# Kernel optimization log

Hardware: AMD Instinct MI355X
Metric: run time of the kernel (lower is better)

Reference implementation:

```python
import jax, jax.numpy as jnp
import numpy as np

MODEL_DIM = 1024
TOTAL_DIM = 1024
N_HEADS = 16
HEAD_DIM = TOTAL_DIM // N_HEADS


def setup_inputs() -> dict:
    key = jax.random.key(0)
    k1, k2, k3 = jax.random.split(key, 3)
    query = jax.random.normal(k1, (2, 2048, MODEL_DIM), dtype=jnp.float32)
    # nn.Linear(model_dim, 3*total_dim, bias=False): store as [in, out] for x @ W
    W_in = jax.random.normal(k2, (MODEL_DIM, 3 * TOTAL_DIM), dtype=jnp.float32) / np.sqrt(MODEL_DIM)
    W_out = jax.random.normal(k3, (TOTAL_DIM, MODEL_DIM), dtype=jnp.float32) / np.sqrt(TOTAL_DIM)
    return {"query": query, "W_in": W_in, "W_out": W_out}


def reference(query, W_in, W_out):
    B, S, _ = query.shape
    qkv = query @ W_in                      # [B, S, 3*D]
    q, k, v = jnp.split(qkv, 3, axis=-1)    # each [B, S, D]

    def to_heads(t):
        return t.reshape(B, S, N_HEADS, HEAD_DIM).transpose(0, 2, 1, 3)  # [B,H,S,d]

    q, k, v = to_heads(q), to_heads(k), to_heads(v)
    scale = 1.0 / np.sqrt(HEAD_DIM).astype(np.float32)
    scores = jnp.einsum('bhqd,bhkd->bhqk', q, k) * scale  # [B,H,S,S]
    causal = jnp.tril(jnp.ones((S, S), dtype=bool))
    scores = jnp.where(causal, scores, jnp.finfo(scores.dtype).min)
    probs = jax.nn.softmax(scores, axis=-1)
    attn = jnp.einsum('bhqk,bhkd->bhqd', probs, v)        # [B,H,S,d]
    attn = attn.transpose(0, 2, 1, 3).reshape(B, S, TOTAL_DIM)
    return attn @ W_out                     # [B, S, model_dim]
```

## Files before the change

kernel.cpp:

```cpp
#include <hip/hip_runtime.h>


typedef __bf16 bf16x8 __attribute__((ext_vector_type(8)));
typedef __bf16 bf16x4 __attribute__((ext_vector_type(4)));
typedef short s16x4 __attribute__((ext_vector_type(4)));
typedef float f32x4 __attribute__((ext_vector_type(4)));
typedef int i32x2 __attribute__((ext_vector_type(2)));

#define B_   2
#define S_   2048
#define DM   1024
#define NH   16
#define HD   64
#define N3   3072
#define M_   4096

#define SCALE_LOG2E 0.180336884f

__device__ __forceinline__ unsigned short f2bf(float f) {
  unsigned int u = __float_as_uint(f);
  u += 0x7fffu + ((u >> 16) & 1u);
  return (unsigned short)(u >> 16);
}

__device__ __forceinline__ void gload_lds16(void* lds, const void* g) {
  __builtin_amdgcn_global_load_lds(
      (__attribute__((address_space(1))) void*)g,
      (__attribute__((address_space(3))) void*)lds, 16, 0, 0);
}

__device__ __forceinline__ f32x4 mfma16(bf16x4 a, bf16x4 b, f32x4 c) {
#if __has_builtin(__builtin_amdgcn_mfma_f32_16x16x16_bf16)
  return __builtin_amdgcn_mfma_f32_16x16x16_bf16(a, b, c, 0, 0, 0);
#else
  return __builtin_amdgcn_mfma_f32_16x16x16bf16_1k(
      __builtin_bit_cast(s16x4, a), __builtin_bit_cast(s16x4, b), c, 0, 0, 0);
#endif
}

__device__ __forceinline__ int cvtpk(float s0, float s1) {
  int r;
  asm("v_cvt_pk_bf16_f32 %0, %1, %2" : "=v"(r) : "v"(s0), "v"(s1));
  return r;
}

__global__ __launch_bounds__(256) void f32_to_bf16_vec(
    const float4* __restrict__ in, unsigned short* __restrict__ out, int n4) {
  int i = blockIdx.x * 256 + threadIdx.x;
  if (i < n4) {
    float4 v = in[i];
    ushort4 o;
    o.x = f2bf(v.x); o.y = f2bf(v.y); o.z = f2bf(v.z); o.w = f2bf(v.w);
    *(ushort4*)(&out[(size_t)i * 4]) = o;
  }
}

__global__ __launch_bounds__(256) void transpose_f32_bf16(
    const float* __restrict__ in, unsigned short* __restrict__ out, int R, int C,
    int scale_rows, float scale) {
  __shared__ float tile[32][33];
  const int tx = threadIdx.x, ty = threadIdx.y;
  const int x = blockIdx.x * 32 + tx;
  const int y0 = blockIdx.y * 32;
#pragma unroll
  for (int j = 0; j < 32; j += 8)
    tile[ty + j][tx] = in[(size_t)(y0 + ty + j) * C + x];
  __syncthreads();
  const int ox = y0 + tx;
  const int oy0 = blockIdx.x * 32;
#pragma unroll
  for (int j = 0; j < 32; j += 8) {
    const int orow = oy0 + ty + j;
    float v = tile[tx][ty + j];
    if (orow < scale_rows) v *= scale;
    out[(size_t)orow * R + ox] = f2bf(v);
  }
}

__global__ __launch_bounds__(256) void transpose_v(
    const unsigned short* __restrict__ qkv, unsigned short* __restrict__ vTn) {
  __shared__ unsigned short tile[64][72];
  const int kt = blockIdx.x;
  const int h  = blockIdx.y;
  const int b  = blockIdx.z;
  const int t  = threadIdx.x;
  const int row = t >> 3;
  const int c8  = (t & 7) * 8;
#pragma unroll
  for (int rr = 0; rr < 2; rr++) {
    const int s = row + rr * 32;
    const size_t src = (size_t)(b * S_ + kt * 64 + s) * N3 + 2 * DM + h * HD + c8;
    *(float4*)&tile[s][c8] = *(const float4*)&qkv[src];
  }
  __syncthreads();
  const size_t base = (size_t)((b * NH + h) * 32 + kt) * 4096;
#pragma unroll
  for (int u0 = 0; u0 < 2; u0++) {
    const int u = t + u0 * 256;
    const int p = u >> 8, d = (u >> 2) & 63, q = u & 3;
    const int s0 = 32 * p + q * 4;
    ushort4 w0, w1;
    w0.x = tile[s0 + 0][d];  w0.y = tile[s0 + 1][d];
    w0.z = tile[s0 + 2][d];  w0.w = tile[s0 + 3][d];
    w1.x = tile[s0 + 16][d]; w1.y = tile[s0 + 17][d];
    w1.z = tile[s0 + 18][d]; w1.w = tile[s0 + 19][d];
    *(ushort4*)&vTn[base + (size_t)u * 8]     = w0;
    *(ushort4*)&vTn[base + (size_t)u * 8 + 4] = w1;
  }
}

template <int OUT_BF16>
__global__ __launch_bounds__(256) void gemm_abt(
    const unsigned short* __restrict__ A, const unsigned short* __restrict__ Bt,
    void* __restrict__ Cv, int M, int N, int K) {
  __shared__ __align__(16) unsigned short a_sm[128 * 32];
  __shared__ __align__(16) unsigned short b_sm[128 * 32];
  const int tid = threadIdx.x;
  const int lane = tid & 63, wave = tid >> 6;
  const int quad = lane >> 4, l15 = lane & 15;
  const int row0 = blockIdx.y * 128, col0 = blockIdx.x * 128;
  const int wm = (wave >> 1) * 64, wn = (wave & 1) * 64;

  f32x4 acc[4][4];
#pragma unroll
  for (int i = 0; i < 4; i++)
#pragma unroll
    for (int j = 0; j < 4; j++) acc[i][j] = (f32x4){0.f, 0.f, 0.f, 0.f};

  const int e0 = tid * 8;

  for (int k0 = 0; k0 < K; k0 += 32) {
    __syncthreads();
#pragma unroll
    for (int i = 0; i < 2; i++) {
      int e = e0 + i * 2048;
      int r = e >> 5, c = e & 31;
      gload_lds16(&a_sm[e], &A[(size_t)(row0 + r) * K + k0 + c]);
      gload_lds16(&b_sm[e], &Bt[(size_t)(col0 + r) * K + k0 + c]);
    }
    __syncthreads();

    bf16x8 af[4], bfb[4];
#pragma unroll
    for (int i = 0; i < 4; i++) {
      af[i]  = *(const bf16x8*)&a_sm[(wm + i * 16 + l15) * 32 + quad * 8];
      bfb[i] = *(const bf16x8*)&b_sm[(wn + i * 16 + l15) * 32 + quad * 8];
    }
#pragma unroll
    for (int i = 0; i < 4; i++)
#pragma unroll
      for (int j = 0; j < 4; j++)
        acc[i][j] = __builtin_amdgcn_mfma_f32_16x16x32_bf16(af[i], bfb[j], acc[i][j], 0, 0, 0);
  }

#pragma unroll
  for (int i = 0; i < 4; i++) {
#pragma unroll
    for (int j = 0; j < 4; j++) {
#pragma unroll
      for (int r = 0; r < 4; r++) {
        const int row = row0 + wm + i * 16 + quad * 4 + r;
        const int col = col0 + wn + j * 16 + l15;
        const float v = acc[i][j][r];
        if (OUT_BF16)
          ((unsigned short*)Cv)[(size_t)row * N + col] = f2bf(v);
        else
          ((float*)Cv)[(size_t)row * N + col] = v;
      }
    }
  }
}

__global__ __launch_bounds__(256) void gemm_abt_64(
    const unsigned short* __restrict__ A, const unsigned short* __restrict__ Bt,
    float* __restrict__ C, int M, int N, int K) {
  __shared__ __align__(16) unsigned short a_sm[64 * 32];
  __shared__ __align__(16) unsigned short b_sm[128 * 32];
  const int tid = threadIdx.x;
  const int lane = tid & 63, wave = tid >> 6;
  const int quad = lane >> 4, l15 = lane & 15;
  const int row0 = blockIdx.y * 64, col0 = blockIdx.x * 128;
  const int wn = wave * 32;

  f32x4 acc[4][2];
#pragma unroll
  for (int i = 0; i < 4; i++)
#pragma unroll
    for (int j = 0; j < 2; j++) acc[i][j] = (f32x4){0.f, 0.f, 0.f, 0.f};

  const int e0 = tid * 8;

  for (int k0 = 0; k0 < K; k0 += 32) {
    __syncthreads();
    {
      const int r = e0 >> 5, c = e0 & 31;
      gload_lds16(&a_sm[e0], &A[(size_t)(row0 + r) * K + k0 + c]);
    }
#pragma unroll
    for (int i = 0; i < 2; i++) {
      int e = e0 + i * 2048;
      int r = e >> 5, c = e & 31;
      gload_lds16(&b_sm[e], &Bt[(size_t)(col0 + r) * K + k0 + c]);
    }
    __syncthreads();

    bf16x8 af[4], bfb[2];
#pragma unroll
    for (int i = 0; i < 4; i++)
      af[i] = *(const bf16x8*)&a_sm[(i * 16 + l15) * 32 + quad * 8];
#pragma unroll
    for (int j = 0; j < 2; j++)
      bfb[j] = *(const bf16x8*)&b_sm[(wn + j * 16 + l15) * 32 + quad * 8];
#pragma unroll
    for (int i = 0; i < 4; i++)
#pragma unroll
      for (int j = 0; j < 2; j++)
        acc[i][j] = __builtin_amdgcn_mfma_f32_16x16x32_bf16(af[i], bfb[j], acc[i][j], 0, 0, 0);
  }

#pragma unroll
  for (int i = 0; i < 4; i++) {
#pragma unroll
    for (int j = 0; j < 2; j++) {
#pragma unroll
      for (int r = 0; r < 4; r++) {
        const int row = row0 + i * 16 + quad * 4 + r;
        const int col = col0 + wn + j * 16 + l15;
        C[(size_t)row * N + col] = acc[i][j][r];
      }
    }
  }
}

__global__ __launch_bounds__(512, 4) void attn_fused12(
    const unsigned short* __restrict__ qkv,
    const unsigned short* __restrict__ vTn,
    unsigned short* __restrict__ attnout) {
  const int h = blockIdx.y, b = blockIdx.z;
  const int j = blockIdx.x;
  const int tid = threadIdx.x;
  const int lane = tid & 63, wave = tid >> 6;
  const int quad = lane >> 4, l15 = lane & 15;
  const int sw = l15 & 7;

  __shared__ __align__(16) unsigned short k_sm[4 * 4096];
  __shared__ __align__(16) unsigned short vt_sm[4 * 4096];

  const int wrow0 = (wave < 4) ? (j * 64 + wave * 16)
                               : ((31 - j) * 64 + (wave - 4) * 16);
  const int qrow = wrow0 + l15;

  bf16x8 qf[2];
  {
    const unsigned short* qp = qkv + (size_t)(b * S_ + qrow) * N3 + h * HD + quad * 8;
    qf[0] = *(const bf16x8*)qp;
    qf[1] = *(const bf16x8*)(qp + 32);
  }

  f32x4 o[4];
#pragma unroll
  for (int n = 0; n < 4; n++) o[n] = (f32x4){0.f, 0.f, 0.f, 0.f};
  float lsum = 0.f;

  const int r0s = tid >> 3;
  const int gch = ((tid & 7) ^ (r0s & 7)) * 8;
  const unsigned short* kgb = qkv + (size_t)(b * S_ + r0s) * N3 + DM + h * HD + gch;
  const unsigned short* vgl = vTn + (size_t)((b * NH + h) * 32) * 4096 + tid * 8;

  const int nt = 32 - j;

  int pk[4][2];
  const unsigned short* vbp = &vt_sm[0];

  auto PV = [&]() {
    __builtin_amdgcn_s_setprio(1);
#pragma unroll
    for (int p = 0; p < 2; p++) {
      i32x2 wlo, whi;
      wlo.x = pk[2 * p][0];     wlo.y = pk[2 * p][1];
      whi.x = pk[2 * p + 1][0]; whi.y = pk[2 * p + 1][1];
      const bf16x4 blo = __builtin_bit_cast(bf16x4, wlo);
      const bf16x4 bhi = __builtin_bit_cast(bf16x4, whi);
#pragma unroll
      for (int mb = 0; mb < 4; mb++) {
        const bf16x8 vv =
            *(const bf16x8*)&vbp[(p * 256 + mb * 64 + l15 * 4 + quad) * 8];
        bf16x4 alo, ahi;
#pragma unroll
        for (int i = 0; i < 4; i++) { alo[i] = vv[i]; ahi[i] = vv[i + 4]; }
        o[mb] = mfma16(alo, blo, o[mb]);
        o[mb] = mfma16(ahi, bhi, o[mb]);
      }
    }
    __builtin_amdgcn_s_setprio(0);
  };

  gload_lds16(&k_sm[tid * 8], kgb);
  gload_lds16(&vt_sm[tid * 8], vgl);
  gload_lds16(&k_sm[4096 + tid * 8], kgb + (size_t)64 * N3);
  gload_lds16(&vt_sm[4096 + tid * 8], vgl + 4096);

  for (int t = 0; t < nt; t++) {
    if (t + 1 < nt) asm volatile("s_waitcnt vmcnt(2)" ::: "memory");
    else            asm volatile("s_waitcnt vmcnt(0)" ::: "memory");
    __builtin_amdgcn_s_barrier();
    __builtin_amdgcn_sched_barrier(0);
    if (t + 2 < nt) {
      const int b2 = (t + 2) & 3;
      gload_lds16(&k_sm[b2 * 4096 + tid * 8], kgb + (size_t)(t + 2) * 64 * N3);
      gload_lds16(&vt_sm[b2 * 4096 + tid * 8], vgl + (size_t)(t + 2) * 4096);
    }
    const unsigned short* kb = &k_sm[(t & 3) * 4096];
    const unsigned short* vb = &vt_sm[(t & 3) * 4096];

    if (t >= 1 && (t - 1) * 64 <= wrow0 + 15) PV();

    if (t * 64 <= wrow0 + 15) {
      f32x4 s[4];
#pragma unroll
      for (int mb = 0; mb < 4; mb++) s[mb] = (f32x4){0.f, 0.f, 0.f, 0.f};
      __builtin_amdgcn_s_setprio(1);
#pragma unroll
      for (int mb = 0; mb < 4; mb++) {
        const int ro = (mb * 16 + l15) * 64;
        bf16x8 kf0 = *(const bf16x8*)&kb[ro + ((quad ^ sw) << 3)];
        bf16x8 kf1 = *(const bf16x8*)&kb[ro + (((4 + quad) ^ sw) << 3)];
        s[mb] = __builtin_amdgcn_mfma_f32_16x16x32_bf16(kf0, qf[0], s[mb], 0, 0, 0);
        s[mb] = __builtin_amdgcn_mfma_f32_16x16x32_bf16(kf1, qf[1], s[mb], 0, 0, 0);
      }
      __builtin_amdgcn_s_setprio(0);

      if (t * 64 + 63 <= wrow0) {
#pragma unroll
        for (int mb = 0; mb < 4; mb++)
#pragma unroll
          for (int r = 0; r < 4; r++)
            s[mb][r] = exp2f(s[mb][r]);
      } else {
        const int kq0 = t * 64 + quad * 4;
#pragma unroll
        for (int mb = 0; mb < 4; mb++)
#pragma unroll
          for (int r = 0; r < 4; r++) {
            const float e = exp2f(s[mb][r]);
            s[mb][r] = (kq0 + mb * 16 + r <= qrow) ? e : 0.f;
          }
      }
#pragma unroll
      for (int mb = 0; mb < 4; mb++)
        lsum += (s[mb][0] + s[mb][1]) + (s[mb][2] + s[mb][3]);

#pragma unroll
      for (int mb = 0; mb < 4; mb++) {
        pk[mb][0] = cvtpk(s[mb][0], s[mb][1]);
        pk[mb][1] = cvtpk(s[mb][2], s[mb][3]);
      }
      vbp = vb;
    }
  }

  if ((nt - 1) * 64 <= wrow0 + 15) PV();

  asm volatile("s_waitcnt vmcnt(0)" ::: "memory");

  float l = lsum;
  l += __shfl_xor(l, 16);
  l += __shfl_xor(l, 32);
  const float inv = 1.0f / l;
  const size_t grow = (size_t)(b * S_ + qrow);
#pragma unroll
  for (int mb = 0; mb < 4; mb++) {
    ushort4 w;
    w.x = f2bf(o[mb][0] * inv);
    w.y = f2bf(o[mb][1] * inv);
    w.z = f2bf(o[mb][2] * inv);
    w.w = f2bf(o[mb][3] * inv);
    *(ushort4*)&attnout[grow * DM + h * HD + mb * 16 + quad * 4] = w;
  }
}

extern "C" void kernel_launch(void* const* d_in, const int* in_sizes, int n_in,
                              void* d_out, int out_size, void* d_ws, size_t ws_size,
                              hipStream_t stream) {
  const float* query = (const float*)d_in[0];
  const float* w_in  = (const float*)d_in[1];
  const float* w_out = (const float*)d_in[2];
  float* out = (float*)d_out;

  char* ws = (char*)d_ws;
  unsigned short* qbf     = (unsigned short*)(ws);
  unsigned short* vTn     = (unsigned short*)(ws);
  unsigned short* w_in_t  = (unsigned short*)(ws + 8388608);
  unsigned short* w_out_t = (unsigned short*)(ws + 14680064);
  unsigned short* qkv     = (unsigned short*)(ws + 16777216);
  unsigned short* attn    = (unsigned short*)(ws + 41943040);

  f32_to_bf16_vec<<<dim3(M_ * DM / 1024), dim3(256), 0, stream>>>(
      (const float4*)query, qbf, M_ * DM / 4);
  transpose_f32_bf16<<<dim3(N3 / 32, DM / 32), dim3(32, 8), 0, stream>>>(
      w_in, w_in_t, DM, N3, DM, SCALE_LOG2E);
  transpose_f32_bf16<<<dim3(DM / 32, DM / 32), dim3(32, 8), 0, stream>>>(
      w_out, w_out_t, DM, DM, 0, 1.0f);
  gemm_abt<1><<<dim3(N3 / 128, M_ / 128), dim3(256), 0, stream>>>(qbf, w_in_t, qkv, M_, N3, DM);
  transpose_v<<<dim3(32, NH, B_), dim3(256), 0, stream>>>(qkv, vTn);
  attn_fused12<<<dim3(16, NH, B_), dim3(512), 0, stream>>>(qkv, vTn, attn);
  gemm_abt_64<<<dim3(DM / 128, M_ / 64), dim3(256), 0, stream>>>(attn, w_out_t, out, M_, DM, DM);
}
```

Baseline: 194.6 us.

## Merge prep kernels and write V transposed directly from QKV GEMM epilogue

Combines the query cast and both weight transposes into a single prep launch that dispatches on block index. The QKV GEMM epilogue now writes the V section straight into the blocked transposed layout used by attention, so the separate transpose_v kernel and its read-back of V are gone. Workspace offsets are reshuffled so attn reuses the qbf region and vTn gets its own buffer. This saves two launches and a V round trip through memory, at the cost of scattered 8-byte stores in the GEMM epilogue.

```diff
diff --git a/kernel.cpp b/kernel.cpp
--- a/kernel.cpp
+++ b/kernel.cpp
@@ -44,75 +44,54 @@
   return r;
 }
 
-__global__ __launch_bounds__(256) void f32_to_bf16_vec(
-    const float4* __restrict__ in, unsigned short* __restrict__ out, int n4) {
-  int i = blockIdx.x * 256 + threadIdx.x;
-  if (i < n4) {
-    float4 v = in[i];
+__global__ __launch_bounds__(256) void prep(
+    const float* __restrict__ query, const float* __restrict__ w_in,
+    const float* __restrict__ w_out, unsigned short* __restrict__ qbf,
+    unsigned short* __restrict__ w_in_t, unsigned short* __restrict__ w_out_t) {
+  __shared__ float tile[32][33];
+  const int bx = blockIdx.x;
+  const int t = threadIdx.x;
+  if (bx < 4096) {
+    const int i = bx * 256 + t;
+    const float4 v = ((const float4*)query)[i];
     ushort4 o;
     o.x = f2bf(v.x); o.y = f2bf(v.y); o.z = f2bf(v.z); o.w = f2bf(v.w);
-    *(ushort4*)(&out[(size_t)i * 4]) = o;
-  }
-}
-
-__global__ __launch_bounds__(256) void transpose_f32_bf16(
-    const float* __restrict__ in, unsigned short* __restrict__ out, int R, int C,
-    int scale_rows, float scale) {
-  __shared__ float tile[32][33];
-  const int tx = threadIdx.x, ty = threadIdx.y;
-  const int x = blockIdx.x * 32 + tx;
-  const int y0 = blockIdx.y * 32;
+    *(ushort4*)(&qbf[(size_t)i * 4]) = o;
+    return;
+  }
+  const int tx = t & 31, ty = t >> 5;
+  const float* in;
+  unsigned short* out;
+  int R, C, bxx, bxy, scale_rows;
+  if (bx < 4096 + 3072) {
+    const int id = bx - 4096;
+    in = w_in; out = w_in_t; R = DM; C = N3;
+    bxx = id % 96; bxy = id / 96; scale_rows = DM;
+  } else {
+    const int id = bx - 7168;
+    in = w_out; out = w_out_t; R = DM; C = DM;
+    bxx = id & 31; bxy = id >> 5; scale_rows = 0;
+  }
+  const int x = bxx * 32 + tx;
+  const int y0 = bxy * 32;
 #pragma unroll
   for (int j = 0; j < 32; j += 8)
     tile[ty + j][tx] = in[(size_t)(y0 + ty + j) * C + x];
   __syncthreads();
   const int ox = y0 + tx;
-  const int oy0 = blockIdx.x * 32;
+  const int oy0 = bxx * 32;
 #pragma unroll
   for (int j = 0; j < 32; j += 8) {
     const int orow = oy0 + ty + j;
     float v = tile[tx][ty + j];
-    if (orow < scale_rows) v *= scale;
+    if (orow < scale_rows) v *= SCALE_LOG2E;
     out[(size_t)orow * R + ox] = f2bf(v);
   }
 }
 
-__global__ __launch_bounds__(256) void transpose_v(
-    const unsigned short* __restrict__ qkv, unsigned short* __restrict__ vTn) {
-  __shared__ unsigned short tile[64][72];
-  const int kt = blockIdx.x;
-  const int h  = blockIdx.y;
-  const int b  = blockIdx.z;
-  const int t  = threadIdx.x;
-  const int row = t >> 3;
-  const int c8  = (t & 7) * 8;
-#pragma unroll
-  for (int rr = 0; rr < 2; rr++) {
-    const int s = row + rr * 32;
-    const size_t src = (size_t)(b * S_ + kt * 64 + s) * N3 + 2 * DM + h * HD + c8;
-    *(float4*)&tile[s][c8] = *(const float4*)&qkv[src];
-  }
-  __syncthreads();
-  const size_t base = (size_t)((b * NH + h) * 32 + kt) * 4096;
-#pragma unroll
-  for (int u0 = 0; u0 < 2; u0++) {
-    const int u = t + u0 * 256;
-    const int p = u >> 8, d = (u >> 2) & 63, q = u & 3;
-    const int s0 = 32 * p + q * 4;
-    ushort4 w0, w1;
-    w0.x = tile[s0 + 0][d];  w0.y = tile[s0 + 1][d];
-    w0.z = tile[s0 + 2][d];  w0.w = tile[s0 + 3][d];
-    w1.x = tile[s0 + 16][d]; w1.y = tile[s0 + 17][d];
-    w1.z = tile[s0 + 18][d]; w1.w = tile[s0 + 19][d];
-    *(ushort4*)&vTn[base + (size_t)u * 8]     = w0;
-    *(ushort4*)&vTn[base + (size_t)u * 8 + 4] = w1;
-  }
-}
-
-template <int OUT_BF16>
-__global__ __launch_bounds__(256) void gemm_abt(
+__global__ __launch_bounds__(256) void gemm_qkv(
     const unsigned short* __restrict__ A, const unsigned short* __restrict__ Bt,
-    void* __restrict__ Cv, int M, int N, int K) {
+    unsigned short* __restrict__ qkv, unsigned short* __restrict__ vTn) {
   __shared__ __align__(16) unsigned short a_sm[128 * 32];
   __shared__ __align__(16) unsigned short b_sm[128 * 32];
   const int tid = threadIdx.x;
@@ -120,6 +99,7 @@
   const int quad = lane >> 4, l15 = lane & 15;
   const int row0 = blockIdx.y * 128, col0 = blockIdx.x * 128;
   const int wm = (wave >> 1) * 64, wn = (wave & 1) * 64;
+  const int K = DM;
 
   f32x4 acc[4][4];
 #pragma unroll
@@ -153,19 +133,39 @@
         acc[i][j] = __builtin_amdgcn_mfma_f32_16x16x32_bf16(af[i], bfb[j], acc[i][j], 0, 0, 0);
   }
 
-#pragma unroll
-  for (int i = 0; i < 4; i++) {
-#pragma unroll
-    for (int j = 0; j < 4; j++) {
-#pragma unroll
-      for (int r = 0; r < 4; r++) {
-        const int row = row0 + wm + i * 16 + quad * 4 + r;
-        const int col = col0 + wn + j * 16 + l15;
-        const float v = acc[i][j][r];
-        if (OUT_BF16)
-          ((unsigned short*)Cv)[(size_t)row * N + col] = f2bf(v);
-        else
-          ((float*)Cv)[(size_t)row * N + col] = v;
+  if (col0 + wn < 2 * DM) {
+#pragma unroll
+    for (int i = 0; i < 4; i++) {
+#pragma unroll
+      for (int j = 0; j < 4; j++) {
+#pragma unroll
+        for (int r = 0; r < 4; r++) {
+          const int row = row0 + wm + i * 16 + quad * 4 + r;
+          const int col = col0 + wn + j * 16 + l15;
+          qkv[(size_t)row * N3 + col] = f2bf(acc[i][j][r]);
+        }
+      }
+    }
+  } else {
+    const int head = (col0 + wn - 2 * DM) >> 6;
+#pragma unroll
+    for (int i = 0; i < 4; i++) {
+      const int row = row0 + wm + i * 16 + quad * 4;
+      const int b = row >> 11;
+      const int srow = row & 2047;
+      const int kt = srow >> 6;
+      const int s = srow & 63;
+      const int p = s >> 5, half = (s >> 4) & 1, q = (s >> 2) & 3;
+      const size_t base = (size_t)((b * NH + head) * 32 + kt) * 4096;
+#pragma unroll
+      for (int j = 0; j < 4; j++) {
+        const int d = j * 16 + l15;
+        ushort4 w;
+        w.x = f2bf(acc[i][j][0]);
+        w.y = f2bf(acc[i][j][1]);
+        w.z = f2bf(acc[i][j][2]);
+        w.w = f2bf(acc[i][j][3]);
+        *(ushort4*)&vTn[base + (size_t)(p * 256 + d * 4 + q) * 8 + half * 4] = w;
       }
     }
   }
@@ -389,20 +389,14 @@
 
   char* ws = (char*)d_ws;
   unsigned short* qbf     = (unsigned short*)(ws);
-  unsigned short* vTn     = (unsigned short*)(ws);
+  unsigned short* attn    = (unsigned short*)(ws);
   unsigned short* w_in_t  = (unsigned short*)(ws + 8388608);
   unsigned short* w_out_t = (unsigned short*)(ws + 14680064);
   unsigned short* qkv     = (unsigned short*)(ws + 16777216);
-  unsigned short* attn    = (unsigned short*)(ws + 41943040);
-
-  f32_to_bf16_vec<<<dim3(M_ * DM / 1024), dim3(256), 0, stream>>>(
-      (const float4*)query, qbf, M_ * DM / 4);
-  transpose_f32_bf16<<<dim3(N3 / 32, DM / 32), dim3(32, 8), 0, stream>>>(
-      w_in, w_in_t, DM, N3, DM, SCALE_LOG2E);
-  transpose_f32_bf16<<<dim3(DM / 32, DM / 32), dim3(32, 8), 0, stream>>>(
-      w_out, w_out_t, DM, DM, 0, 1.0f);
-  gemm_abt<1><<<dim3(N3 / 128, M_ / 128), dim3(256), 0, stream>>>(qbf, w_in_t, qkv, M_, N3, DM);
-  transpose_v<<<dim3(32, NH, B_), dim3(256), 0, stream>>>(qkv, vTn);
+  unsigned short* vTn     = (unsigned short*)(ws + 41943040);
+
+  prep<<<dim3(8192), dim3(256), 0, stream>>>(query, w_in, w_out, qbf, w_in_t, w_out_t);
+  gemm_qkv<<<dim3(N3 / 128, M_ / 128), dim3(256), 0, stream>>>(qbf, w_in_t, qkv, vTn);
   attn_fused12<<<dim3(16, NH, B_), dim3(512), 0, stream>>>(qkv, vTn, attn);
   gemm_abt_64<<<dim3(DM / 128, M_ / 64), dim3(256), 0, stream>>>(attn, w_out_t, out, M_, DM, DM);
 }
```

After: 192.7 us. No clear change (-1.0%).
